# Optimization experiments

Measured on AMD Instinct MI355X. Metric: run time of the kernel, lower is better.

The kernel has to match this reference:

```python
import jax, jax.numpy as jnp
import numpy as np

NUM_PERGROUP = 32
EPS = 0.001


def setup_inputs() -> dict:
    key = jax.random.key(0)
    k1, k2, k3, k4 = jax.random.split(key, 4)
    N, C, H, W = 8, 256, 128, 128
    ncls = 3
    x = jax.random.normal(k1, (N, C, H, W), dtype=jnp.float32)
    class_id = jax.random.randint(k2, (N,), 0, ncls, dtype=jnp.int64)
    # xavier_uniform-ish scale for embedkernel rows (each row is a CxC matrix)
    limit = float(np.sqrt(6.0 / (ncls + C * C)))
    embedkernel = jax.random.uniform(k3, (ncls, C * C), dtype=jnp.float32,
                                     minval=-limit, maxval=limit)
    embedbias = jnp.zeros((ncls, C), dtype=jnp.float32)
    conv_w = jax.random.normal(k4, (C, C, 1, 1), dtype=jnp.float32) * (1.0 / np.sqrt(C))
    conv_b = jax.random.normal(jax.random.fold_in(key, 5), (C,), dtype=jnp.float32) * 0.01
    return {"x": x, "class_id": class_id, "embedkernel": embedkernel,
            "embedbias": embedbias, "conv_w": conv_w, "conv_b": conv_b}


def _whiten(x):
    N, C, H, W = x.shape
    c = NUM_PERGROUP
    g = C // c
    xf = x.reshape(N * g, c, H * W)          # (N*g, c, HW)
    m = xf.mean(-1, keepdims=True)
    f = xf - m
    cov = jnp.matmul(f, jnp.swapaxes(f, 1, 2)) / (H * W)   # (N*g, c, c)
    cov = (1.0 - EPS) * cov + EPS * jnp.eye(c, dtype=x.dtype)
    L = jnp.linalg.cholesky(cov)             # lower-triangular, matches torch.cholesky
    inv_sqrt = jnp.linalg.inv(L)
    f_hat = jnp.matmul(inv_sqrt, f)
    return f_hat.reshape(N, C, H, W)


def _color(x, class_id, embedkernel, embedbias, conv_w, conv_b):
    N, C, H, W = x.shape
    w = conv_w[:, :, 0, 0]                   # (Cout, Cin)
    uncond = jnp.einsum('bchw,dc->bdhw', x, w) + conv_b[None, :, None, None]
    kernel = embedkernel[class_id].reshape(N, C, C)   # per-sample CxC
    bias = embedbias[class_id]                        # (N, C)
    xp = x.reshape(N, C, H * W)
    # cond[b,d,p] = sum_c x[b,c,p] * kernel[b,c,d]
    cond = jnp.einsum('bcp,bcd->bdp', xp, kernel).reshape(N, C, H, W)
    cond = cond + bias[:, :, None, None]
    return cond + uncond


def reference(x, class_id, embedkernel, embedbias, conv_w, conv_b):
    xw = _whiten(x)
    return _color(xw, class_id, embedkernel, embedbias, conv_w, conv_b)
```

## Files before the change

kernel.cpp:

```cpp
#include <hip/hip_runtime.h>

typedef unsigned short ushort_t;
typedef __attribute__((ext_vector_type(8)))  short  short8;
typedef __attribute__((ext_vector_type(8)))  ushort_t ushort8;
typedef __attribute__((ext_vector_type(16))) float  f32x16;

#define HWPX 16384
#define EPSV 0.001f

__device__ __forceinline__ ushort_t f2bf(float f) {
    unsigned u = __builtin_bit_cast(unsigned, f);
    unsigned r = u + 0x7FFFu + ((u >> 16) & 1u);
    return (ushort_t)(r >> 16);
}

__device__ __forceinline__ unsigned cvt_pk(float a, float b) {
    unsigned r;
    asm("v_cvt_pk_bf16_f32 %0, %1, %2" : "=v"(r) : "v"(a), "v"(b));
    return r;
}

__device__ __forceinline__ void gld_lds16(const ushort_t* g, ushort_t* l) {
    __builtin_amdgcn_global_load_lds(
        (const __attribute__((address_space(1))) unsigned int*)g,
        (__attribute__((address_space(3))) unsigned int*)l, 16, 0, 0);
}

__device__ __forceinline__ void stats_load(float4 (&buf)[4], const float* xbase,
                                           int w, int col4, int sub) {
    #pragma unroll
    for (int rr = 0; rr < 4; ++rr)
        buf[rr] = *(const float4*)(xbase + (size_t)(w + rr * 8) * HWPX + sub * 256 + col4 * 4);
}

template<bool XBF>
__global__ __launch_bounds__(512, 4) void k_stats(const float* __restrict__ x,
                                                  float* __restrict__ part,
                                                  ushort_t* __restrict__ xbt) {
    __shared__ char smraw[40960];
    ushort_t* tile = (ushort_t*)smraw;
    float (*redc)[1024] = (float(*)[1024])smraw;
    float (*redm)[64] = (float(*)[64])(smraw + 32768);
    int b = blockIdx.x;
    int n = b >> 6, g = (b >> 3) & 7, q = b & 7;
    int t = threadIdx.x, w = t >> 6, l = t & 63;
    int lo = l & 31, hi = l >> 5, col4 = l;
    const float* xbase = x + ((size_t)(n * 256 + g * 32)) * HWPX + q * 2048;

    f32x16 acc = {};
    float sm[4] = {0.f, 0.f, 0.f, 0.f};
    float4 buf[4], nxt[4];

    stats_load(buf, xbase, w, col4, 0);
    #pragma unroll 1
    for (int s = 0; s < 8; ++s) {
        if (s < 7) stats_load(nxt, xbase, w, col4, s + 1);
        ushort_t* tl = tile + (s & 1) * 8192;
        #pragma unroll
        for (int rr = 0; rr < 4; ++rr) {
            float4 v = buf[rr];
            sm[rr] += v.x + v.y + v.z + v.w;
            uint2 u;
            u.x = cvt_pk(v.x, v.y);
            u.y = cvt_pk(v.z, v.w);
            int row = w + rr * 8;
            int idx = (row * 256 + col4 * 4) ^ ((row & 7) << 3);
            *(uint2*)&tl[idx] = u;
        }
        asm volatile("s_waitcnt lgkmcnt(0)" ::: "memory");
        __builtin_amdgcn_s_barrier();
        __builtin_amdgcn_sched_barrier(0);
        #pragma unroll
        for (int ks2 = 0; ks2 < 2; ++ks2) {
            int pidx = (lo * 256 + w * 32 + ks2 * 16 + hi * 8) ^ ((lo & 7) << 3);
            short8 f = *(const short8*)&tl[pidx];
            acc = __builtin_amdgcn_mfma_f32_32x32x16_bf16(f, f, acc, 0, 0, 0);
        }
        if (XBF) {
            int pb = q * 64 + s * 8 + w;
            #pragma unroll
            for (int h = 0; h < 2; ++h) {
                ushort8 o;
                #pragma unroll
                for (int j = 0; j < 8; ++j) {
                    int c = h * 16 + hi * 8 + j;
                    o[j] = tl[(c * 256 + w * 32 + lo) ^ ((c & 7) << 3)];
                }
                *(ushort8*)(xbt + ((((size_t)(n * 512 + pb)) * 16 + g * 2 + h) * 64 + l) * 8) = o;
            }
        }
        #pragma unroll
        for (int rr = 0; rr < 4; ++rr) buf[rr] = nxt[rr];
    }

    __syncthreads();
    #pragma unroll
    for (int r = 0; r < 16; ++r) redc[w][l * 16 + r] = acc[r];
    #pragma unroll
    for (int rr = 0; rr < 4; ++rr) redm[w + rr * 8][col4] = sm[rr];
    __syncthreads();

    for (int i = t; i < 1024; i += 512) {
        float v = 0.f;
        #pragma unroll
        for (int ww = 0; ww < 8; ++ww) v += redc[ww][i];
        int ll = i >> 4, r = i & 15;
        int row = (r & 3) + 8 * (r >> 2) + 4 * (ll >> 5);
        int col = ll & 31;
        part[(size_t)b * 1056 + row * 32 + col] = v;
    }
    if (t < 32) {
        float v = 0.f;
        for (int c = 0; c < 64; ++c) v += redm[t][c];
        part[(size_t)b * 1056 + 1024 + t] = v;
    }
}

template<bool FRAG>
__global__ __launch_bounds__(256, 1) void k_prep(const float* __restrict__ part,
                                                 const float* __restrict__ conv_w,
                                                 const float* __restrict__ EK,
                                                 const int* __restrict__ cls_arr,
                                                 ushort_t* __restrict__ M_bf,
                                                 float* __restrict__ bp) {
    int bid = blockIdx.x;
    int n = bid >> 3, g = bid & 7;
    int t = threadIdx.x;
    __shared__ float cov[1024];
    __shared__ float sums[32];
    __shared__ float A[32][33];
    __shared__ float ml[32];
    __shared__ float cw[256][33];

    for (int i = 0; i < 8; ++i) {
        int r = i * 32 + (t >> 3);
        float4 v = *(const float4*)(conv_w + r * 256 + g * 32 + (t & 7) * 4);
        #pragma unroll
        for (int e = 0; e < 4; ++e) cw[r][(t & 7) * 4 + e] = ((float*)&v)[e];
    }

    for (int i = t; i < 1024; i += 256) {
        float v = 0.f;
        for (int q = 0; q < 8; ++q) v += part[(size_t)(bid * 8 + q) * 1056 + i];
        cov[i] = v;
    }
    if (t < 32) {
        float v = 0.f;
        for (int q = 0; q < 8; ++q) v += part[(size_t)(bid * 8 + q) * 1056 + 1024 + t];
        sums[t] = v;
    }
    __syncthreads();

    const float invHW = 1.0f / (float)HWPX;
    #pragma unroll
    for (int p = 0; p < 4; ++p) {
        int idx = t + p * 256;
        int r = idx >> 5, c = idx & 31;
        float mr = sums[r] * invHW, mc = sums[c] * invHW;
        A[r][c] = (cov[idx] * invHW - mr * mc) * (1.0f - EPSV) + ((r == c) ? EPSV : 0.f);
    }
    if (t < 32) ml[t] = sums[t] * invHW;
    __syncthreads();

    int d = t;
    int cls = cls_arr[n];
    float a[32];
    #pragma unroll
    for (int c = 0; c < 32; ++c)
        a[c] = cw[d][c] + EK[(size_t)cls * 65536 + (size_t)(g * 32 + c) * 256 + d];

    for (int k = 0; k < 30; k += 2) {
        float d0 = A[k][k];
        float invd0 = 1.0f / d0;
        float r10 = A[k + 1][k] * invd0;
        float d1 = A[k + 1][k + 1] - A[k + 1][k] * r10;
        float invd1 = 1.0f / d1;
        #pragma unroll
        for (int p = 0; p < 4; ++p) {
            int idx = t + p * 256;
            int i = idx >> 5, j = idx & 31;
            if (j > k + 1 && j <= i) {
                float aik = A[i][k], ajk = A[j][k];
                float ai1 = A[i][k + 1] - aik * r10;
                float aj1 = A[j][k + 1] - ajk * r10;
                A[i][j] = A[i][j] - aik * ajk * invd0 - ai1 * aj1 * invd1;
            }
        }
        __syncthreads();
    }
    {
        float vals[4], dsq[4];
        #pragma unroll
        for (int p = 0; p < 4; ++p) {
            int idx = t + p * 256;
            int i = idx >> 5, j = idx & 31;
            float v, dj;
            if (j & 1) {
                float r = A[j][j - 1] / A[j - 1][j - 1];
                dj = A[j][j] - A[j][j - 1] * r;
                v  = A[i][j] - A[i][j - 1] * r;
            } else {
                dj = A[j][j];
                v  = A[i][j];
            }
            vals[p] = v;
            dsq[p] = sqrtf(dj);
        }
        __syncthreads();
        #pragma unroll
        for (int p = 0; p < 4; ++p) {
            int idx = t + p * 256;
            int i = idx >> 5, j = idx & 31;
            if (j <= i) A[i][j] = vals[p] / dsq[p];
        }
        __syncthreads();
    }

    float m[32];
    #pragma unroll
    for (int j = 31; j >= 0; --j) {
        float s = a[j];
        #pragma unroll
        for (int cp = j + 1; cp < 32; ++cp) s -= m[cp] * A[cp][j];
        m[j] = s / A[j][j];
    }

    float bpv = 0.f;
    ushort8 pk[4];
    #pragma unroll
    for (int cp = 0; cp < 32; ++cp) {
        bpv += m[cp] * ml[cp];
        pk[cp >> 3][cp & 7] = f2bf(m[cp]);
    }
    if (FRAG) {
        #pragma unroll
        for (int kk = 0; kk < 4; ++kk) {
            size_t u = (((size_t)(n * 8 + (d >> 5)) * 16) + g * 2 + (kk >> 1)) * 64
                       + (d & 31) + 32 * (kk & 1);
            *(ushort8*)(M_bf + u * 8) = pk[kk];
        }
    } else {
        ushort_t* dst = M_bf + ((size_t)(n * 256 + d)) * 256 + g * 32;
        #pragma unroll
        for (int k = 0; k < 4; ++k) *(ushort8*)(dst + k * 8) = pk[k];
    }
    bp[(size_t)(n * 8 + g) * 256 + d] = bpv;
}

__global__ __launch_bounds__(256) void k_bias(const float* __restrict__ conv_b,
                                              const float* __restrict__ EB,
                                              const int* __restrict__ cls_arr,
                                              const float* __restrict__ bp,
                                              float* __restrict__ bias) {
    int n = blockIdx.x, d = threadIdx.x;
    int cls = cls_arr[n];
    float v = conv_b[d] + EB[cls * 256 + d];
    #pragma unroll
    for (int g = 0; g < 8; ++g) v -= bp[(size_t)(n * 8 + g) * 256 + d];
    bias[n * 256 + d] = v;
}

__global__ __launch_bounds__(512, 4) void k_gemm_s(const ushort_t* __restrict__ xbt,
                                                   const ushort_t* __restrict__ M_t,
                                                   const float* __restrict__ conv_b,
                                                   const float* __restrict__ EB,
                                                   const int* __restrict__ cls_arr,
                                                   const float* __restrict__ bp,
                                                   float* __restrict__ out) {
    __shared__ ushort_t bstage[32768];
    __shared__ float bias_l[256];
    int bid = blockIdx.x;
    int n = bid >> 6, pt = bid & 63;
    int t = threadIdx.x, w = t >> 6, l = t & 63, lo = l & 31, hi = l >> 5;
    int dblk = w * 32;

    if (t < 256) {
        int cls = cls_arr[n];
        float v = conv_b[t] + EB[cls * 256 + t];
        #pragma unroll
        for (int g = 0; g < 8; ++g) v -= bp[(size_t)(n * 8 + g) * 256 + t];
        bias_l[t] = v;
    }

    const ushort_t* msrc = M_t + (((size_t)(n * 8 + w) * 16) * 64 + l) * 8;
    short8 a[16];
    #pragma unroll
    for (int ks = 0; ks < 16; ++ks)
        a[ks] = *(const short8*)(msrc + (size_t)ks * 512);

    const ushort_t* xsrc = xbt + (size_t)(n * 512 + pt * 8) * 8192;

    #pragma unroll
    for (int p = 0; p < 3; ++p) {
        const ushort_t* src = xsrc + (size_t)p * 8192;
        gld_lds16(src + w * 1024 + l * 8,       bstage + p * 8192 + w * 1024);
        gld_lds16(src + w * 1024 + 512 + l * 8, bstage + p * 8192 + w * 1024 + 512);
    }
    asm volatile("s_waitcnt vmcnt(4) lgkmcnt(0)" ::: "memory");
    __builtin_amdgcn_s_barrier();
    __builtin_amdgcn_sched_barrier(0);

    float4 bsv4[4];
    #pragma unroll
    for (int qq = 0; qq < 4; ++qq)
        bsv4[qq] = *(const float4*)&bias_l[dblk + 8 * qq + 4 * hi];

    #pragma unroll 1
    for (int pb = 0; pb < 8; ++pb) {
        ushort_t* bufc = bstage + (pb & 3) * 8192;
        if (pb + 3 < 8) {
            ushort_t* bufn = bstage + ((pb + 3) & 3) * 8192;
            const ushort_t* src = xsrc + (size_t)(pb + 3) * 8192;
            gld_lds16(src + w * 1024 + l * 8,       bufn + w * 1024);
            gld_lds16(src + w * 1024 + 512 + l * 8, bufn + w * 1024 + 512);
        }
        __builtin_amdgcn_sched_barrier(0);

        f32x16 acc = {};
        #pragma unroll
        for (int ks = 0; ks < 16; ++ks) {
            short8 bf = *(const short8*)(bufc + ks * 512 + l * 8);
            acc = __builtin_amdgcn_mfma_f32_32x32x16_bf16(a[ks], bf, acc, 0, 0, 0);
        }

        int px = (pt * 8 + pb) * 32 + lo;
        #pragma unroll
        for (int r = 0; r < 16; ++r) {
            int row = dblk + (r & 3) + 8 * (r >> 2) + 4 * hi;
            out[((size_t)(n * 256 + row)) * HWPX + px] =
                acc[r] + ((const float*)&bsv4[r >> 2])[r & 3];
        }

        if (pb < 7) {
            if (pb == 0)      asm volatile("s_waitcnt vmcnt(20)" ::: "memory");
            else if (pb == 1) asm volatile("s_waitcnt vmcnt(36)" ::: "memory");
            else if (pb < 5)  asm volatile("s_waitcnt vmcnt(52)" ::: "memory");
            else if (pb == 5) asm volatile("s_waitcnt vmcnt(50)" ::: "memory");
            else              asm volatile("s_waitcnt vmcnt(48)" ::: "memory");
            __builtin_amdgcn_sched_barrier(0);
            __builtin_amdgcn_s_barrier();
            __builtin_amdgcn_sched_barrier(0);
        }
    }
}

__global__ __launch_bounds__(512, 2) void k_gemm_fb(const float* __restrict__ x,
                                                    const ushort_t* __restrict__ M_bf,
                                                    const float* __restrict__ bias,
                                                    float* __restrict__ out) {
    int bid = blockIdx.x;
    int n = bid >> 8, pt = bid & 255;
    int px0 = pt * 64;
    int t = threadIdx.x, w = t >> 6, l = t & 63, lo = l & 31, hi = l >> 5;
    int dblk = w * 32;

    const ushort_t* Mrow = M_bf + ((size_t)(n * 256 + dblk + lo)) * 256;
    const float* xn = x + (size_t)n * 256 * HWPX;

    f32x16 acc0 = {}, acc1 = {};
    for (int ks = 0; ks < 16; ++ks) {
        int c0 = ks * 16 + hi * 8;
        short8 afrag = *(const short8*)(Mrow + c0);
        const float* xc = xn + (size_t)c0 * HWPX + px0 + lo;
        short8 f0, f1;
        #pragma unroll
        for (int bb = 0; bb < 8; ++bb) {
            f0[bb] = (short)f2bf(xc[(size_t)bb * HWPX]);
            f1[bb] = (short)f2bf(xc[(size_t)bb * HWPX + 32]);
        }
        acc0 = __builtin_amdgcn_mfma_f32_32x32x16_bf16(afrag, f0, acc0, 0, 0, 0);
        acc1 = __builtin_amdgcn_mfma_f32_32x32x16_bf16(afrag, f1, acc1, 0, 0, 0);
    }

    #pragma unroll
    for (int r = 0; r < 16; ++r) {
        int row = dblk + (r & 3) + 8 * (r >> 2) + 4 * hi;
        float bs = bias[n * 256 + row];
        size_t o = ((size_t)(n * 256 + row)) * HWPX + px0 + lo;
        out[o] = acc0[r] + bs;
        out[o + 32] = acc1[r] + bs;
    }
}

extern "C" void kernel_launch(void* const* d_in, const int* in_sizes, int n_in,
                              void* d_out, int out_size, void* d_ws, size_t ws_size,
                              hipStream_t stream) {
    const float* x      = (const float*)d_in[0];
    const int*   cls    = (const int*)d_in[1];
    const float* EK     = (const float*)d_in[2];
    const float* EB     = (const float*)d_in[3];
    const float* conv_w = (const float*)d_in[4];
    const float* conv_b = (const float*)d_in[5];
    float* out = (float*)d_out;

    float* wsf   = (float*)d_ws;
    float* part  = wsf;
    float* bp    = wsf + 540672;
    float* bias  = wsf + 557056;
    ushort_t* M  = (ushort_t*)(wsf + 559104);

    const size_t xb_off   = 559104 * sizeof(float) + (size_t)8 * 256 * 256 * 2;
    const size_t xb_bytes = (size_t)8 * HWPX * 256 * 2;
    bool fast = ws_size >= xb_off + xb_bytes;
    ushort_t* xb = (ushort_t*)((char*)d_ws + xb_off);

    if (fast) {
        k_stats<true>  <<<512, 512, 0, stream>>>(x, part, xb);
        k_prep<true>   <<<64,  256, 0, stream>>>(part, conv_w, EK, cls, M, bp);
        k_gemm_s       <<<512, 512, 0, stream>>>(xb, M, conv_b, EB, cls, bp, out);
    } else {
        k_stats<false> <<<512, 512, 0, stream>>>(x, part, M);
        k_prep<false>  <<<64,  256, 0, stream>>>(part, conv_w, EK, cls, M, bp);
        k_bias         <<<8,   256, 0, stream>>>(conv_b, EB, cls, bp, bias);
        k_gemm_fb      <<<2048, 512, 0, stream>>>(x, M, bias, out);
    }
}
```

Baseline: 99.22 us.

## Fuse whitening-matrix prep into stats kernel via last-block atomic counter

Folds the per-group Cholesky, triangular solve and bf16 packing of the combined colour matrix into the tail of the stats kernel. The last of the eight blocks for each (sample, group) is detected with an atomic counter and does the work. This removes a separate k_prep launch and its dependency gap on the fast path. In exchange it adds a memset, threadfences and a serial tail on 64 blocks, plus extra register pressure in the stats kernel, which could lower occupancy.

```diff
diff --git a/kernel.cpp b/kernel.cpp
--- a/kernel.cpp
+++ b/kernel.cpp
@@ -36,8 +36,15 @@
 template<bool XBF>
 __global__ __launch_bounds__(512, 4) void k_stats(const float* __restrict__ x,
                                                   float* __restrict__ part,
-                                                  ushort_t* __restrict__ xbt) {
+                                                  ushort_t* __restrict__ xbt,
+                                                  unsigned* __restrict__ cnt,
+                                                  const float* __restrict__ conv_w,
+                                                  const float* __restrict__ EK,
+                                                  const int* __restrict__ cls_arr,
+                                                  ushort_t* __restrict__ M_bf,
+                                                  float* __restrict__ bp) {
     __shared__ char smraw[40960];
+    __shared__ unsigned last;
     ushort_t* tile = (ushort_t*)smraw;
     float (*redc)[1024] = (float(*)[1024])smraw;
     float (*redm)[64] = (float(*)[64])(smraw + 32768);
@@ -113,6 +120,128 @@
         float v = 0.f;
         for (int c = 0; c < 64; ++c) v += redm[t][c];
         part[(size_t)b * 1056 + 1024 + t] = v;
+    }
+
+    if (!XBF) return;
+
+    __syncthreads();
+    if (t == 0) {
+        __threadfence();
+        last = atomicAdd(&cnt[(n << 3) + g], 1u);
+    }
+    __syncthreads();
+    if (last != 7u) return;
+    __threadfence();
+
+    float* cov2     = (float*)smraw;
+    float (*A2)[33] = (float(*)[33])(smraw + 4096);
+    float* sums2    = (float*)(smraw + 8448);
+    float* ml2      = (float*)(smraw + 8576);
+    int bg = (n << 3) + g;
+
+    for (int i = t; i < 1024; i += 512) {
+        float v = 0.f;
+        for (int qq = 0; qq < 8; ++qq) v += part[(size_t)(bg * 8 + qq) * 1056 + i];
+        cov2[i] = v;
+    }
+    if (t < 32) {
+        float v = 0.f;
+        for (int qq = 0; qq < 8; ++qq) v += part[(size_t)(bg * 8 + qq) * 1056 + 1024 + t];
+        sums2[t] = v;
+    }
+    __syncthreads();
+
+    const float invHW = 1.0f / (float)HWPX;
+    #pragma unroll
+    for (int p = 0; p < 2; ++p) {
+        int idx = t + p * 512;
+        int r = idx >> 5, c = idx & 31;
+        float mr = sums2[r] * invHW, mc = sums2[c] * invHW;
+        A2[r][c] = (cov2[idx] * invHW - mr * mc) * (1.0f - EPSV) + ((r == c) ? EPSV : 0.f);
+    }
+    if (t < 32) ml2[t] = sums2[t] * invHW;
+    __syncthreads();
+
+    int d = t;
+    int cls = cls_arr[n];
+    float av[32];
+    if (t < 256) {
+        #pragma unroll
+        for (int c = 0; c < 32; ++c)
+            av[c] = conv_w[d * 256 + g * 32 + c]
+                  + EK[(size_t)cls * 65536 + (size_t)(g * 32 + c) * 256 + d];
+    }
+
+    for (int k = 0; k < 30; k += 2) {
+        float d0 = A2[k][k];
+        float invd0 = 1.0f / d0;
+        float r10 = A2[k + 1][k] * invd0;
+        float d1 = A2[k + 1][k + 1] - A2[k + 1][k] * r10;
+        float invd1 = 1.0f / d1;
+        #pragma unroll
+        for (int p = 0; p < 2; ++p) {
+            int idx = t + p * 512;
+            int i = idx >> 5, j = idx & 31;
+            if (j > k + 1 && j <= i) {
+                float aik = A2[i][k], ajk = A2[j][k];
+                float ai1 = A2[i][k + 1] - aik * r10;
+                float aj1 = A2[j][k + 1] - ajk * r10;
+                A2[i][j] = A2[i][j] - aik * ajk * invd0 - ai1 * aj1 * invd1;
+            }
+        }
+        __syncthreads();
+    }
+    {
+        float vals[2], dsq[2];
+        #pragma unroll
+        for (int p = 0; p < 2; ++p) {
+            int idx = t + p * 512;
+            int i = idx >> 5, j = idx & 31;
+            float v, dj;
+            if (j & 1) {
+                float r = A2[j][j - 1] / A2[j - 1][j - 1];
+                dj = A2[j][j] - A2[j][j - 1] * r;
+                v  = A2[i][j] - A2[i][j - 1] * r;
+            } else {
+                dj = A2[j][j];
+                v  = A2[i][j];
+            }
+            vals[p] = v;
+            dsq[p] = sqrtf(dj);
+        }
+        __syncthreads();
+        #pragma unroll
+        for (int p = 0; p < 2; ++p) {
+            int idx = t + p * 512;
+            int i = idx >> 5, j = idx & 31;
+            if (j <= i) A2[i][j] = vals[p] / dsq[p];
+        }
+        __syncthreads();
+    }
+
+    if (t < 256) {
+        float m[32];
+        #pragma unroll
+        for (int j = 31; j >= 0; --j) {
+            float s2 = av[j];
+            #pragma unroll
+            for (int cp = j + 1; cp < 32; ++cp) s2 -= m[cp] * A2[cp][j];
+            m[j] = s2 / A2[j][j];
+        }
+        float bpv = 0.f;
+        ushort8 pk[4];
+        #pragma unroll
+        for (int cp = 0; cp < 32; ++cp) {
+            bpv += m[cp] * ml2[cp];
+            pk[cp >> 3][cp & 7] = f2bf(m[cp]);
+        }
+        #pragma unroll
+        for (int kk = 0; kk < 4; ++kk) {
+            size_t u = (((size_t)(n * 8 + (d >> 5)) * 16) + g * 2 + (kk >> 1)) * 64
+                       + (d & 31) + 32 * (kk & 1);
+            *(ushort8*)(M_bf + u * 8) = pk[kk];
+        }
+        bp[(size_t)bg * 256 + d] = bpv;
     }
 }
 
@@ -393,23 +522,26 @@
     const float* conv_b = (const float*)d_in[5];
     float* out = (float*)d_out;
 
-    float* wsf   = (float*)d_ws;
-    float* part  = wsf;
-    float* bp    = wsf + 540672;
-    float* bias  = wsf + 557056;
-    ushort_t* M  = (ushort_t*)(wsf + 559104);
-
-    const size_t xb_off   = 559104 * sizeof(float) + (size_t)8 * 256 * 256 * 2;
+    float* wsf      = (float*)d_ws;
+    float* part     = wsf;
+    float* bp       = wsf + 540672;
+    float* bias     = wsf + 557056;
+    unsigned* cnt   = (unsigned*)(wsf + 559104);
+    ushort_t* M     = (ushort_t*)(wsf + 559168);
+
+    const size_t xb_off   = 559168 * sizeof(float) + (size_t)8 * 256 * 256 * 2;
     const size_t xb_bytes = (size_t)8 * HWPX * 256 * 2;
     bool fast = ws_size >= xb_off + xb_bytes;
     ushort_t* xb = (ushort_t*)((char*)d_ws + xb_off);
 
     if (fast) {
-        k_stats<true>  <<<512, 512, 0, stream>>>(x, part, xb);
-        k_prep<true>   <<<64,  256, 0, stream>>>(part, conv_w, EK, cls, M, bp);
+        hipMemsetAsync(cnt, 0, 64 * sizeof(unsigned), stream);
+        k_stats<true>  <<<512, 512, 0, stream>>>(x, part, xb, cnt,
+                                                 conv_w, EK, cls, M, bp);
         k_gemm_s       <<<512, 512, 0, stream>>>(xb, M, conv_b, EB, cls, bp, out);
     } else {
-        k_stats<false> <<<512, 512, 0, stream>>>(x, part, M);
+        k_stats<false> <<<512, 512, 0, stream>>>(x, part, M, nullptr,
+                                                 conv_w, EK, cls, M, bp);
         k_prep<false>  <<<64,  256, 0, stream>>>(part, conv_w, EK, cls, M, bp);
         k_bias         <<<8,   256, 0, stream>>>(conv_b, EB, cls, bp, bias);
         k_gemm_fb      <<<2048, 512, 0, stream>>>(x, M, bias, out);
```

After: 196.9 us. +98.5%, slower.
